# Optimization experiments

Hardware: AMD Instinct MI355X
Metric: run time of the kernel (lower is better)

Reference implementation:

```python
import jax, jax.numpy as jnp
import numpy as np

B, L, HID = 4, 1024, 1024
H, D = 16, 64  # num heads, head size


def setup_inputs() -> dict:
    key = jax.random.key(0)
    ks = jax.random.split(key, 12)
    s = 0.02
    return {
        "hidden_states": jax.random.normal(ks[0], (B, L, HID), jnp.float32),
        "attention_mask": jnp.zeros((B, 1, 1, L), jnp.float32),
        "structure_matrix": jax.random.normal(ks[1], (L, L, D), jnp.float32),
        # torch nn.Linear weights are [out, in]
        "Wq": jax.random.normal(ks[2], (H * D, HID), jnp.float32) * s,
        "bq": jnp.zeros((H * D,), jnp.float32),
        "Wk": jax.random.normal(ks[3], (H * D, HID), jnp.float32) * s,
        "bk": jnp.zeros((H * D,), jnp.float32),
        "Wv": jax.random.normal(ks[4], (H * D, HID), jnp.float32) * s,
        "bv": jnp.zeros((H * D,), jnp.float32),
        "Wsq": jax.random.normal(ks[5], (D, D), jnp.float32) * s,
        "bsq": jnp.zeros((D,), jnp.float32),
        "Wsk": jax.random.normal(ks[6], (D, D), jnp.float32) * s,
        "bsk": jnp.zeros((D,), jnp.float32),
    }


def _heads(x):
    # [B, L, H*D] -> [B, H, L, D]
    return x.reshape(B, L, H, D).transpose(0, 2, 1, 3)


def reference(hidden_states, attention_mask, structure_matrix,
              Wq, bq, Wk, bk, Wv, bv, Wsq, bsq, Wsk, bsk):
    q = _heads(hidden_states @ Wq.T + bq)  # [B,H,L,D]
    k = _heads(hidden_states @ Wk.T + bk)
    v = _heads(hidden_states @ Wv.T + bv)

    scores = jnp.einsum('bhld,bhrd->bhlr', q, k)

    sq = structure_matrix @ Wsq.T + bsq  # [L,L,D]
    sk = structure_matrix @ Wsk.T + bsk
    scores = scores + jnp.einsum('bhld,lrd->bhlr', q, sq) \
                    + jnp.einsum('bhrd,lrd->bhlr', k, sk)

    scores = scores / jnp.sqrt(jnp.float32(D)) + attention_mask
    probs = jax.nn.softmax(scores, axis=-1)
    ctx = jnp.einsum('bhlr,bhrd->bhld', probs, v)
    ctx = ctx.transpose(0, 2, 1, 3).reshape(B, L, H * D)
    return ctx, scores
```

## Files before the change

kernel.cpp:

```cpp
#include <hip/hip_runtime.h>

typedef __attribute__((ext_vector_type(8))) short short8v;
typedef __attribute__((ext_vector_type(4))) short short4v;
typedef __attribute__((ext_vector_type(4))) float float4v;
typedef __attribute__((ext_vector_type(2))) unsigned int uint2v;

#define MFMA16(a,b,c) __builtin_amdgcn_mfma_f32_16x16x32_bf16(a,b,c,0,0,0)

__device__ __forceinline__ unsigned short f2b(float f) {
    union { float f; unsigned u; } v; v.f = f;
    unsigned r = v.u + 0x7FFFu + ((v.u >> 16) & 1u);
    return (unsigned short)(r >> 16);
}
__device__ __forceinline__ float b2f(unsigned short s) {
    union { unsigned u; float f; } v; v.u = ((unsigned)s) << 16;
    return v.f;
}
__device__ __forceinline__ short8v pack8(float4v a, float4v b) {
    union { unsigned u[4]; short8v s; } o;
    asm("v_cvt_pk_bf16_f32 %0, %1, %2" : "=v"(o.u[0]) : "v"(a[0]), "v"(a[1]));
    asm("v_cvt_pk_bf16_f32 %0, %1, %2" : "=v"(o.u[1]) : "v"(a[2]), "v"(a[3]));
    asm("v_cvt_pk_bf16_f32 %0, %1, %2" : "=v"(o.u[2]) : "v"(b[0]), "v"(b[1]));
    asm("v_cvt_pk_bf16_f32 %0, %1, %2" : "=v"(o.u[3]) : "v"(b[2]), "v"(b[3]));
    return o.s;
}

__global__ __launch_bounds__(256) void pack_all(
    const float* __restrict__ hidden, const float* __restrict__ Wq,
    const float* __restrict__ Wk, const float* __restrict__ Wv,
    unsigned short* __restrict__ hb, unsigned short* __restrict__ Wqb,
    unsigned short* __restrict__ Wkb, unsigned short* __restrict__ Wvb) {
    const int bid = blockIdx.x;
    const float* in; unsigned short* out; int i;
    if (bid < 2048)      { in = hidden; out = hb;  i = bid * 256 + threadIdx.x; }
    else if (bid < 2560) { in = Wq; out = Wqb; i = (bid - 2048) * 256 + threadIdx.x; }
    else if (bid < 3072) { in = Wk; out = Wkb; i = (bid - 2560) * 256 + threadIdx.x; }
    else                 { in = Wv; out = Wvb; i = (bid - 3072) * 256 + threadIdx.x; }
    float4v a = *(const float4v*)&in[(size_t)i * 8];
    float4v b = *(const float4v*)&in[(size_t)i * 8 + 4];
    *(short8v*)&out[(size_t)i * 8] = pack8(a, b);
}

__global__ __launch_bounds__(256) void qkv_gemm(
    const unsigned short* __restrict__ A,
    const unsigned short* __restrict__ Wqb, const unsigned short* __restrict__ Wkb,
    const unsigned short* __restrict__ Wvb,
    const float* __restrict__ bq, const float* __restrict__ bk,
    const float* __restrict__ bv,
    unsigned short* __restrict__ outq) {
    const int n0g = blockIdx.x * 64;
    const int which = n0g >> 10;
    const int n0 = n0g & 1023;
    const unsigned short* W = (which == 0) ? Wqb : (which == 1) ? Wkb : Wvb;
    const float* bias = (which == 0) ? bq : (which == 1) ? bk : bv;
    unsigned short* out = outq + (size_t)which * 4194304;
    const int vmode = (which == 2);
    const int wave = threadIdx.x >> 6, lane = threadIdx.x & 63;
    const int m0 = blockIdx.y * 128 + wave * 32;
    const int lrow = lane & 15, g8 = (lane >> 4) << 3, row4 = (lane >> 4) << 2;
    float4v acc[2][4] = {};
    const unsigned short* Ap = A + (size_t)(m0 + lrow) * 1024 + g8;
    const unsigned short* Wp = W + (size_t)(n0 + lrow) * 1024 + g8;
#pragma unroll 2
    for (int k0 = 0; k0 < 1024; k0 += 32) {
        short8v a0 = *(const short8v*)(Ap + k0);
        short8v a1 = *(const short8v*)(Ap + 16 * 1024 + k0);
        short8v b0 = *(const short8v*)(Wp + k0);
        short8v b1 = *(const short8v*)(Wp + 16 * 1024 + k0);
        short8v b2 = *(const short8v*)(Wp + 32 * 1024 + k0);
        short8v b3 = *(const short8v*)(Wp + 48 * 1024 + k0);
        acc[0][0] = MFMA16(a0, b0, acc[0][0]); acc[0][1] = MFMA16(a0, b1, acc[0][1]);
        acc[0][2] = MFMA16(a0, b2, acc[0][2]); acc[0][3] = MFMA16(a0, b3, acc[0][3]);
        acc[1][0] = MFMA16(a1, b0, acc[1][0]); acc[1][1] = MFMA16(a1, b1, acc[1][1]);
        acc[1][2] = MFMA16(a1, b2, acc[1][2]); acc[1][3] = MFMA16(a1, b3, acc[1][3]);
    }
#pragma unroll
    for (int nt = 0; nt < 4; ++nt) {
        const int n = n0 + nt * 16 + lrow;
        const float bz = bias[n];
        const int h = n >> 6, d = n & 63;
#pragma unroll
        for (int mt = 0; mt < 2; ++mt) {
            const int mb = m0 + mt * 16 + row4;
            if (vmode == 0) {
#pragma unroll
                for (int j = 0; j < 4; ++j) {
                    const int m = mb + j;
                    const int b = m >> 10, l = m & 1023;
                    out[(((size_t)(b * 16 + h) << 10) + l) * 64 + d] = f2b(acc[mt][nt][j] + bz);
                }
            } else {
                const int b = mb >> 10, r = mb & 1023;
                short4v pk;
#pragma unroll
                for (int j = 0; j < 4; ++j) pk[j] = (short)f2b(acc[mt][nt][j] + bz);
                *(short4v*)&out[((((size_t)(b * 16 + h)) << 6) + d) * 1024 + r] = pk;
            }
        }
    }
}

__global__ __launch_bounds__(256) void headproj(
    const unsigned short* __restrict__ xh,
    const float* __restrict__ Wsx,
    const float* __restrict__ bsx,
    unsigned short* __restrict__ x2b,
    float* __restrict__ xbv) {
    __shared__ __align__(16) float Ws[64 * 64];
    __shared__ float bs[64];
    __shared__ __align__(16) unsigned short Xl[64 * 64];
    const int tid = threadIdx.x;
    const int l = blockIdx.x;
#pragma unroll
    for (int i = 0; i < 4; ++i)
        *(float4v*)&Ws[tid * 4 + i * 1024] = *(const float4v*)&Wsx[tid * 4 + i * 1024];
    if (tid < 64) bs[tid] = bsx[tid];
    {
        const int bhh = tid >> 2, dq = (tid & 3) * 16;
        const unsigned short* src = &xh[((size_t)bhh * 1024 + l) * 64 + dq];
        *(short8v*)&Xl[bhh * 64 + dq] = *(const short8v*)src;
        *(short8v*)&Xl[bhh * 64 + dq + 8] = *(const short8v*)(src + 8);
    }
    __syncthreads();
    const int bh = tid >> 2, e0 = (tid & 3) * 16;
    float acc[16] = {};
    float bacc = 0.f;
    for (int d = 0; d < 64; ++d) {
        const float xd = b2f(Xl[bh * 64 + d]);
        bacc += xd * bs[d];
        const float* wr = &Ws[d * 64 + e0];
#pragma unroll
        for (int e = 0; e < 16; e += 4) {
            float4v w = *(const float4v*)&wr[e];
            acc[e] += xd * w[0]; acc[e + 1] += xd * w[1];
            acc[e + 2] += xd * w[2]; acc[e + 3] += xd * w[3];
        }
    }
    short8v p0, p1;
#pragma unroll
    for (int e = 0; e < 8; ++e) { p0[e] = (short)f2b(acc[e]); p1[e] = (short)f2b(acc[e + 8]); }
    unsigned short* dst = &x2b[((size_t)l * 64 + bh) * 64 + e0];
    *(short8v*)dst = p0; *(short8v*)(dst + 8) = p1;
    if ((tid & 3) == 0) xbv[l * 64 + bh] = bacc;
}

__global__ __launch_bounds__(256, 4) void struct_fused(
    const float* __restrict__ S,
    const unsigned short* __restrict__ q2b,
    const unsigned short* __restrict__ k2b,
    const float* __restrict__ qbv,
    const float* __restrict__ kbv,
    unsigned short* __restrict__ sb) {
    __shared__ __align__(16) unsigned short Ssh[256 * 64];
    __shared__ __align__(16) unsigned short t3g[4][4][16][16];
    const int tid = threadIdx.x;
    const int w = tid >> 6, lane = tid & 63;
    const int lrow = lane & 15, g = lane >> 4;
    const int g8 = g << 3, row4 = g << 2;
    const int w16 = w << 4;
    const int r0 = blockIdx.x << 4, l0 = blockIdx.y << 4;

    {
        const int u = tid & 15, roff = tid >> 4;
        const float* gp = S + ((size_t)l0 * 1024 + r0 + roff) * 64 + u * 4;
        float4v f[16];
#pragma unroll
        for (int i = 0; i < 16; ++i)
            f[i] = *(const float4v*)(gp + (size_t)i * 65536);
#pragma unroll
        for (int i = 0; i < 16; ++i) {
            const int R = (i << 4) + roff;
            const int K3 = (roff ^ i) & 7;
            const int pu = u ^ (K3 << 1);
            union { unsigned uu[2]; uint2v v2; } o;
            asm("v_cvt_pk_bf16_f32 %0, %1, %2" : "=v"(o.uu[0]) : "v"(f[i][0]), "v"(f[i][1]));
            asm("v_cvt_pk_bf16_f32 %0, %1, %2" : "=v"(o.uu[1]) : "v"(f[i][2]), "v"(f[i][3]));
            *(uint2v*)&Ssh[(R << 6) + (pu << 2)] = o.v2;
        }
    }
    float kbreg[4];
#pragma unroll
    for (int j = 0; j < 4; ++j)
        kbreg[j] = kbv[(size_t)(r0 + row4 + j) * 64 + w16 + lrow];
    __syncthreads();

    float4v c3[16];
#pragma unroll
    for (int ri = 0; ri < 16; ++ri) {
        const int row = lrow * 16 + ri;
        const int key = (lrow ^ ri) & 7;
        short8v a0 = *(const short8v*)&Ssh[row * 64 + ((g ^ key) << 3)];
        short8v a1 = *(const short8v*)&Ssh[row * 64 + (((4 + g) ^ key) << 3)];
        const unsigned short* Bp = k2b + ((size_t)(r0 + ri) * 64 + w16 + lrow) * 64 + g8;
        short8v b0 = *(const short8v*)Bp;
        short8v b1 = *(const short8v*)(Bp + 32);
        float4v acc = {};
        acc = MFMA16(a0, b0, acc);
        acc = MFMA16(a1, b1, acc);
        c3[ri] = acc;
    }

#pragma unroll
    for (int G = 0; G < 4; ++G) {
        if (g == G) {
#pragma unroll
            for (int j = 0; j < 4; ++j) {
                float4v la{c3[0][j], c3[1][j], c3[2][j], c3[3][j]};
                float4v lb{c3[4][j], c3[5][j], c3[6][j], c3[7][j]};
                float4v ha{c3[8][j], c3[9][j], c3[10][j], c3[11][j]};
                float4v hb{c3[12][j], c3[13][j], c3[14][j], c3[15][j]};
                *(short8v*)&t3g[w][j][lrow][0] = pack8(la, lb);
                *(short8v*)&t3g[w][j][lrow][8] = pack8(ha, hb);
            }
        }
        asm volatile("s_waitcnt lgkmcnt(0)" ::: "memory");
#pragma unroll
        for (int lj = 0; lj < 4; ++lj) {
            const int li = (G << 2) + lj;
            const int row = li * 16 + lrow;
            const int key = (li ^ lrow) & 7;
            short8v a0 = *(const short8v*)&Ssh[row * 64 + ((g ^ key) << 3)];
            short8v a1 = *(const short8v*)&Ssh[row * 64 + (((4 + g) ^ key) << 3)];
            const unsigned short* Bp = q2b + ((size_t)(l0 + li) * 64 + w16 + lrow) * 64 + g8;
            short8v b0 = *(const short8v*)Bp;
            short8v b1 = *(const short8v*)(Bp + 32);
            float4v c2 = {};
            c2 = MFMA16(a0, b0, c2);
            c2 = MFMA16(a1, b1, c2);
            short4v t3v = *(const short4v*)&t3g[w][lj][lrow][row4];
            const float qb = qbv[(size_t)(l0 + li) * 64 + w16 + lrow];
            short4v outv;
#pragma unroll
            for (int j = 0; j < 4; ++j)
                outv[j] = (short)f2b(c2[j] + b2f((unsigned short)t3v[j]) + qb + kbreg[j]);
            *(short4v*)&sb[((size_t)(l0 + li) * 64 + w16 + lrow) * 1024 + r0 + row4] = outv;
        }
    }
}

__global__ __launch_bounds__(256) void flash_kernel(
    const unsigned short* __restrict__ qh,
    const unsigned short* __restrict__ kh,
    const unsigned short* __restrict__ vT,
    const unsigned short* __restrict__ sb,
    const float* __restrict__ mask,
    float* __restrict__ scores,
    float* __restrict__ ctx) {
    __shared__ __align__(16) unsigned short pL[2][4][2][16][64];
    const int bid = blockIdx.x;
    const int bh  = (bid & 7) * 8 + ((bid >> 3) & 7);
    const int seg = bid >> 6;
    const int tid = threadIdx.x, w = tid >> 6, lane = tid & 63;
    const int l0 = ((seg << 2) | w) << 5;
    const int b = bh >> 4, h = bh & 15;
    const int lam = lane & 15, g = lane >> 4, g8 = g << 3, g4 = g << 2;
    const int key = (lam & 7) << 1;

    short8v qf[2][2];
#pragma unroll
    for (int mt = 0; mt < 2; ++mt)
#pragma unroll
        for (int ks = 0; ks < 2; ++ks)
            qf[mt][ks] = *(const short8v*)&qh[((size_t)bh * 1024 + l0 + mt * 16 + lam) * 64 + ks * 32 + g8];
    const int myl[2] = { l0 + lam, l0 + 16 + lam };
    float mrun[2] = { -3e38f, -3e38f }, sden[2] = { 0.f, 0.f };
    float4v opv[2][4] = {};

    for (int rt = 0; rt < 16; ++rt) {
        const int r0 = rt << 6;
        const int pc = rt & 1;
        float4v sacc[2][4] = {};
#pragma unroll
        for (int rs = 0; rs < 4; ++rs)
#pragma unroll
            for (int ks = 0; ks < 2; ++ks) {
                short8v kf = *(const short8v*)&kh[((size_t)bh * 1024 + r0 + rs * 16 + lam) * 64 + ks * 32 + g8];
                sacc[0][rs] = MFMA16(kf, qf[0][ks], sacc[0][rs]);
                sacc[1][rs] = MFMA16(kf, qf[1][ks], sacc[1][rs]);
            }
        float s8[2][4][4];
        float mx[2] = { -3e38f, -3e38f };
#pragma unroll
        for (int rs = 0; rs < 4; ++rs) {
            float4v mk = *(const float4v*)&mask[(size_t)b * 1024 + r0 + rs * 16 + g4];
#pragma unroll
            for (int mt = 0; mt < 2; ++mt) {
                short4v sbv = *(const short4v*)&sb[((size_t)myl[mt] * 64 + bh) * 1024 + r0 + rs * 16 + g4];
                float4v o;
#pragma unroll
                for (int j = 0; j < 4; ++j) {
                    const float v = (sacc[mt][rs][j] + b2f((unsigned short)sbv[j])) * 0.125f + mk[j];
                    s8[mt][rs][j] = v; o[j] = v;
                    mx[mt] = fmaxf(mx[mt], v);
                }
                *(float4v*)&scores[((size_t)bh * 1024 + myl[mt]) * 1024 + r0 + rs * 16 + g4] = o;
            }
        }
#pragma unroll
        for (int mt = 0; mt < 2; ++mt) {
            float t = mx[mt];
            t = fmaxf(t, __shfl_xor(t, 16));
            t = fmaxf(t, __shfl_xor(t, 32));
            const float mn = fmaxf(mrun[mt], t);
            const float f = __expf(mrun[mt] - mn);
            mrun[mt] = mn;
            float ps = 0.f;
#pragma unroll
            for (int rs = 0; rs < 4; ++rs)
#pragma unroll
                for (int j = 0; j < 4; ++j) {
                    const float p = __expf(s8[mt][rs][j] - mn);
                    s8[mt][rs][j] = p; ps += p;
                }
            ps += __shfl_xor(ps, 16);
            ps += __shfl_xor(ps, 32);
            sden[mt] = sden[mt] * f + ps;
#pragma unroll
            for (int dt = 0; dt < 4; ++dt)
#pragma unroll
                for (int j = 0; j < 4; ++j) opv[mt][dt][j] *= f;
        }
#pragma unroll
        for (int mt = 0; mt < 2; ++mt)
#pragma unroll
            for (int rs = 0; rs < 4; ++rs) {
                union { unsigned uu[2]; uint2v v2; } o;
                asm("v_cvt_pk_bf16_f32 %0, %1, %2" : "=v"(o.uu[0]) : "v"(s8[mt][rs][0]), "v"(s8[mt][rs][1]));
                asm("v_cvt_pk_bf16_f32 %0, %1, %2" : "=v"(o.uu[1]) : "v"(s8[mt][rs][2]), "v"(s8[mt][rs][3]));
                const int unit = ((rs << 2) | g) ^ key;
                *(uint2v*)&pL[pc][w][mt][lam][unit << 2] = o.v2;
            }
#pragma unroll
        for (int ks = 0; ks < 2; ++ks) {
            const int u = (((ks << 3) | (g << 1)) ^ key) << 2;
            short8v pb0 = *(const short8v*)&pL[pc][w][0][lam][u];
            short8v pb1 = *(const short8v*)&pL[pc][w][1][lam][u];
#pragma unroll
            for (int dt = 0; dt < 4; ++dt) {
                short8v va = *(const short8v*)&vT[((size_t)bh * 64 + dt * 16 + lam) * 1024 + r0 + ks * 32 + g8];
                opv[0][dt] = MFMA16(va, pb0, opv[0][dt]);
                opv[1][dt] = MFMA16(va, pb1, opv[1][dt]);
            }
        }
    }
#pragma unroll
    for (int mt = 0; mt < 2; ++mt) {
        const float inv = 1.f / sden[mt];
#pragma unroll
        for (int dt = 0; dt < 4; ++dt) {
            float4v o;
#pragma unroll
            for (int j = 0; j < 4; ++j) o[j] = opv[mt][dt][j] * inv;
            *(float4v*)&ctx[((size_t)b * 1024 + myl[mt]) * 1024 + h * 64 + dt * 16 + g4] = o;
        }
    }
}

extern "C" void kernel_launch(void* const* d_in, const int* in_sizes, int n_in,
                              void* d_out, int out_size, void* d_ws, size_t ws_size,
                              hipStream_t stream) {
    (void)in_sizes; (void)n_in; (void)out_size; (void)ws_size;
    const float* hidden = (const float*)d_in[0];
    const float* mask   = (const float*)d_in[1];
    const float* S      = (const float*)d_in[2];
    const float* Wq  = (const float*)d_in[3];  const float* bq  = (const float*)d_in[4];
    const float* Wk  = (const float*)d_in[5];  const float* bk  = (const float*)d_in[6];
    const float* Wv  = (const float*)d_in[7];  const float* bv  = (const float*)d_in[8];
    const float* Wsq = (const float*)d_in[9];  const float* bsq = (const float*)d_in[10];
    const float* Wsk = (const float*)d_in[11]; const float* bsk = (const float*)d_in[12];

    float* ctx    = (float*)d_out;
    float* scores = ctx + (size_t)4 * 1024 * 1024;

    char* ws = (char*)d_ws;
    unsigned short* sbuf = (unsigned short*)ws;
    unsigned short* hb  = (unsigned short*)ws;
    unsigned short* Wqb = (unsigned short*)(ws + (8u << 20));
    unsigned short* Wkb = (unsigned short*)(ws + (10u << 20));
    unsigned short* Wvb = (unsigned short*)(ws + (12u << 20));
    unsigned short* qh  = (unsigned short*)(ws + (size_t)(128u) * 1024 * 1024);
    unsigned short* kh  = qh  + (size_t)4 * 1024 * 1024;
    unsigned short* vT  = kh  + (size_t)4 * 1024 * 1024;
    unsigned short* q2b = vT  + (size_t)4 * 1024 * 1024;
    unsigned short* k2b = q2b + (size_t)4 * 1024 * 1024;
    float* qbv = (float*)(k2b + (size_t)4 * 1024 * 1024);
    float* kbv = qbv + 65536;

    pack_all<<<3584, 256, 0, stream>>>(hidden, Wq, Wk, Wv, hb, Wqb, Wkb, Wvb);
    qkv_gemm<<<dim3(48, 32), 256, 0, stream>>>(hb, Wqb, Wkb, Wvb, bq, bk, bv, qh);
    headproj<<<1024, 256, 0, stream>>>(qh, Wsq, bsq, q2b, qbv);
    headproj<<<1024, 256, 0, stream>>>(kh, Wsk, bsk, k2b, kbv);
    struct_fused<<<dim3(64, 64), 256, 0, stream>>>(S, q2b, k2b, qbv, kbv, sbuf);
    flash_kernel<<<512, 256, 0, stream>>>(qh, kh, vT, sbuf, mask, scores, ctx);
}
```

Before: 539.1 us.

## Retile structure kernel to 32 l-rows per block and halve flash query tile

```diff
diff --git a/kernel.cpp b/kernel.cpp
--- a/kernel.cpp
+++ b/kernel.cpp
@@ -144,32 +144,33 @@
     if ((tid & 3) == 0) xbv[l * 64 + bh] = bacc;
 }
 
-__global__ __launch_bounds__(256, 4) void struct_fused(
+__global__ __launch_bounds__(256, 2) void struct_fused(
     const float* __restrict__ S,
     const unsigned short* __restrict__ q2b,
     const unsigned short* __restrict__ k2b,
     const float* __restrict__ qbv,
     const float* __restrict__ kbv,
     unsigned short* __restrict__ sb) {
-    __shared__ __align__(16) unsigned short Ssh[256 * 64];
+    __shared__ __align__(16) unsigned short Ssh[512 * 64];
     __shared__ __align__(16) unsigned short t3g[4][4][16][16];
     const int tid = threadIdx.x;
     const int w = tid >> 6, lane = tid & 63;
     const int lrow = lane & 15, g = lane >> 4;
     const int g8 = g << 3, row4 = g << 2;
-    const int w16 = w << 4;
-    const int r0 = blockIdx.x << 4, l0 = blockIdx.y << 4;
-
-    {
+    const int lh = w >> 1, bhh = w & 1;
+    const int r0 = blockIdx.x << 4, l0 = blockIdx.y << 5;
+
+#pragma unroll
+    for (int ph = 0; ph < 2; ++ph) {
         const int u = tid & 15, roff = tid >> 4;
-        const float* gp = S + ((size_t)l0 * 1024 + r0 + roff) * 64 + u * 4;
+        const float* gp = S + ((size_t)(l0 + ph * 16) * 1024 + r0 + roff) * 64 + u * 4;
         float4v f[16];
 #pragma unroll
         for (int i = 0; i < 16; ++i)
             f[i] = *(const float4v*)(gp + (size_t)i * 65536);
 #pragma unroll
         for (int i = 0; i < 16; ++i) {
-            const int R = (i << 4) + roff;
+            const int R = ph * 256 + (i << 4) + roff;
             const int K3 = (roff ^ i) & 7;
             const int pu = u ^ (K3 << 1);
             union { unsigned uu[2]; uint2v v2; } o;
@@ -178,67 +179,71 @@
             *(uint2v*)&Ssh[(R << 6) + (pu << 2)] = o.v2;
         }
     }
-    float kbreg[4];
-#pragma unroll
-    for (int j = 0; j < 4; ++j)
-        kbreg[j] = kbv[(size_t)(r0 + row4 + j) * 64 + w16 + lrow];
     __syncthreads();
 
-    float4v c3[16];
-#pragma unroll
-    for (int ri = 0; ri < 16; ++ri) {
-        const int row = lrow * 16 + ri;
-        const int key = (lrow ^ ri) & 7;
-        short8v a0 = *(const short8v*)&Ssh[row * 64 + ((g ^ key) << 3)];
-        short8v a1 = *(const short8v*)&Ssh[row * 64 + (((4 + g) ^ key) << 3)];
-        const unsigned short* Bp = k2b + ((size_t)(r0 + ri) * 64 + w16 + lrow) * 64 + g8;
-        short8v b0 = *(const short8v*)Bp;
-        short8v b1 = *(const short8v*)(Bp + 32);
-        float4v acc = {};
-        acc = MFMA16(a0, b0, acc);
-        acc = MFMA16(a1, b1, acc);
-        c3[ri] = acc;
-    }
-
-#pragma unroll
-    for (int G = 0; G < 4; ++G) {
-        if (g == G) {
-#pragma unroll
-            for (int j = 0; j < 4; ++j) {
-                float4v la{c3[0][j], c3[1][j], c3[2][j], c3[3][j]};
-                float4v lb{c3[4][j], c3[5][j], c3[6][j], c3[7][j]};
-                float4v ha{c3[8][j], c3[9][j], c3[10][j], c3[11][j]};
-                float4v hb{c3[12][j], c3[13][j], c3[14][j], c3[15][j]};
-                *(short8v*)&t3g[w][j][lrow][0] = pack8(la, lb);
-                *(short8v*)&t3g[w][j][lrow][8] = pack8(ha, hb);
-            }
-        }
-        asm volatile("s_waitcnt lgkmcnt(0)" ::: "memory");
-#pragma unroll
-        for (int lj = 0; lj < 4; ++lj) {
-            const int li = (G << 2) + lj;
-            const int row = li * 16 + lrow;
-            const int key = (li ^ lrow) & 7;
+#pragma unroll
+    for (int bhg = 0; bhg < 2; ++bhg) {
+        const int bhb = bhh * 32 + bhg * 16;
+        float kbreg[4];
+#pragma unroll
+        for (int j = 0; j < 4; ++j)
+            kbreg[j] = kbv[(size_t)(r0 + row4 + j) * 64 + bhb + lrow];
+        float4v c3[16];
+#pragma unroll
+        for (int ri = 0; ri < 16; ++ri) {
+            const int row = lh * 256 + lrow * 16 + ri;
+            const int key = (ri ^ lrow) & 7;
             short8v a0 = *(const short8v*)&Ssh[row * 64 + ((g ^ key) << 3)];
             short8v a1 = *(const short8v*)&Ssh[row * 64 + (((4 + g) ^ key) << 3)];
-            const unsigned short* Bp = q2b + ((size_t)(l0 + li) * 64 + w16 + lrow) * 64 + g8;
+            const unsigned short* Bp = k2b + ((size_t)(r0 + ri) * 64 + bhb + lrow) * 64 + g8;
             short8v b0 = *(const short8v*)Bp;
             short8v b1 = *(const short8v*)(Bp + 32);
-            float4v c2 = {};
-            c2 = MFMA16(a0, b0, c2);
-            c2 = MFMA16(a1, b1, c2);
-            short4v t3v = *(const short4v*)&t3g[w][lj][lrow][row4];
-            const float qb = qbv[(size_t)(l0 + li) * 64 + w16 + lrow];
-            short4v outv;
-#pragma unroll
-            for (int j = 0; j < 4; ++j)
-                outv[j] = (short)f2b(c2[j] + b2f((unsigned short)t3v[j]) + qb + kbreg[j]);
-            *(short4v*)&sb[((size_t)(l0 + li) * 64 + w16 + lrow) * 1024 + r0 + row4] = outv;
-        }
-    }
-}
-
-__global__ __launch_bounds__(256) void flash_kernel(
+            float4v acc = {};
+            acc = MFMA16(a0, b0, acc);
+            acc = MFMA16(a1, b1, acc);
+            c3[ri] = acc;
+        }
+#pragma unroll
+        for (int G = 0; G < 4; ++G) {
+            if (g == G) {
+#pragma unroll
+                for (int j = 0; j < 4; ++j) {
+                    float4v la{c3[0][j], c3[1][j], c3[2][j], c3[3][j]};
+                    float4v lb{c3[4][j], c3[5][j], c3[6][j], c3[7][j]};
+                    float4v ha{c3[8][j], c3[9][j], c3[10][j], c3[11][j]};
+                    float4v hb{c3[12][j], c3[13][j], c3[14][j], c3[15][j]};
+                    *(short8v*)&t3g[w][j][lrow][0] = pack8(la, lb);
+                    *(short8v*)&t3g[w][j][lrow][8] = pack8(ha, hb);
+                }
+            }
+            asm volatile("s_waitcnt lgkmcnt(0)" ::: "memory");
+#pragma unroll
+            for (int lj = 0; lj < 4; ++lj) {
+                const int li = (G << 2) + lj;
+                const int l = l0 + lh * 16 + li;
+                const int row = lh * 256 + li * 16 + lrow;
+                const int key = (li ^ lrow) & 7;
+                short8v a0 = *(const short8v*)&Ssh[row * 64 + ((g ^ key) << 3)];
+                short8v a1 = *(const short8v*)&Ssh[row * 64 + (((4 + g) ^ key) << 3)];
+                const unsigned short* Bp = q2b + ((size_t)l * 64 + bhb + lrow) * 64 + g8;
+                short8v b0 = *(const short8v*)Bp;
+                short8v b1 = *(const short8v*)(Bp + 32);
+                float4v c2 = {};
+                c2 = MFMA16(a0, b0, c2);
+                c2 = MFMA16(a1, b1, c2);
+                short4v t3v = *(const short4v*)&t3g[w][lj][lrow][row4];
+                const float qb = qbv[(size_t)l * 64 + bhb + lrow];
+                short4v outv;
+#pragma unroll
+                for (int j = 0; j < 4; ++j)
+                    outv[j] = (short)f2b(c2[j] + b2f((unsigned short)t3v[j]) + qb + kbreg[j]);
+                *(short4v*)&sb[((size_t)l * 64 + bhb + lrow) * 1024 + r0 + row4] = outv;
+            }
+        }
+    }
+}
+
+__global__ __launch_bounds__(256, 4) void flash_kernel(
     const unsigned short* __restrict__ qh,
     const unsigned short* __restrict__ kh,
     const unsigned short* __restrict__ vT,
@@ -246,112 +251,104 @@
     const float* __restrict__ mask,
     float* __restrict__ scores,
     float* __restrict__ ctx) {
-    __shared__ __align__(16) unsigned short pL[2][4][2][16][64];
+    __shared__ __align__(16) unsigned short pL[2][4][16][64];
     const int bid = blockIdx.x;
     const int bh  = (bid & 7) * 8 + ((bid >> 3) & 7);
     const int seg = bid >> 6;
     const int tid = threadIdx.x, w = tid >> 6, lane = tid & 63;
-    const int l0 = ((seg << 2) | w) << 5;
+    const int l0 = ((seg << 2) | w) << 4;
     const int b = bh >> 4, h = bh & 15;
     const int lam = lane & 15, g = lane >> 4, g8 = g << 3, g4 = g << 2;
     const int key = (lam & 7) << 1;
 
-    short8v qf[2][2];
-#pragma unroll
-    for (int mt = 0; mt < 2; ++mt)
-#pragma unroll
-        for (int ks = 0; ks < 2; ++ks)
-            qf[mt][ks] = *(const short8v*)&qh[((size_t)bh * 1024 + l0 + mt * 16 + lam) * 64 + ks * 32 + g8];
-    const int myl[2] = { l0 + lam, l0 + 16 + lam };
-    float mrun[2] = { -3e38f, -3e38f }, sden[2] = { 0.f, 0.f };
-    float4v opv[2][4] = {};
+    short8v qf[2];
+#pragma unroll
+    for (int ks = 0; ks < 2; ++ks)
+        qf[ks] = *(const short8v*)&qh[((size_t)bh * 1024 + l0 + lam) * 64 + ks * 32 + g8];
+    const int myl = l0 + lam;
+    float mrun = -3e38f, sden = 0.f;
+    float4v opv[4] = {};
 
     for (int rt = 0; rt < 16; ++rt) {
         const int r0 = rt << 6;
         const int pc = rt & 1;
-        float4v sacc[2][4] = {};
+        float4v sacc[4] = {};
+        __builtin_amdgcn_s_setprio(1);
 #pragma unroll
         for (int rs = 0; rs < 4; ++rs)
 #pragma unroll
             for (int ks = 0; ks < 2; ++ks) {
                 short8v kf = *(const short8v*)&kh[((size_t)bh * 1024 + r0 + rs * 16 + lam) * 64 + ks * 32 + g8];
-                sacc[0][rs] = MFMA16(kf, qf[0][ks], sacc[0][rs]);
-                sacc[1][rs] = MFMA16(kf, qf[1][ks], sacc[1][rs]);
-            }
-        float s8[2][4][4];
-        float mx[2] = { -3e38f, -3e38f };
+                sacc[rs] = MFMA16(kf, qf[ks], sacc[rs]);
+            }
+        __builtin_amdgcn_s_setprio(0);
+        float s8[4][4];
+        float mx = -3e38f;
 #pragma unroll
         for (int rs = 0; rs < 4; ++rs) {
             float4v mk = *(const float4v*)&mask[(size_t)b * 1024 + r0 + rs * 16 + g4];
-#pragma unroll
-            for (int mt = 0; mt < 2; ++mt) {
-                short4v sbv = *(const short4v*)&sb[((size_t)myl[mt] * 64 + bh) * 1024 + r0 + rs * 16 + g4];
-                float4v o;
-#pragma unroll
-                for (int j = 0; j < 4; ++j) {
-                    const float v = (sacc[mt][rs][j] + b2f((unsigned short)sbv[j])) * 0.125f + mk[j];
-                    s8[mt][rs][j] = v; o[j] = v;
-                    mx[mt] = fmaxf(mx[mt], v);
-                }
-                *(float4v*)&scores[((size_t)bh * 1024 + myl[mt]) * 1024 + r0 + rs * 16 + g4] = o;
-            }
-        }
-#pragma unroll
-        for (int mt = 0; mt < 2; ++mt) {
-            float t = mx[mt];
+            short4v sbv = *(const short4v*)&sb[((size_t)myl * 64 + bh) * 1024 + r0 + rs * 16 + g4];
+            float4v o;
+#pragma unroll
+            for (int j = 0; j < 4; ++j) {
+                const float v = (sacc[rs][j] + b2f((unsigned short)sbv[j])) * 0.125f + mk[j];
+                s8[rs][j] = v; o[j] = v;
+                mx = fmaxf(mx, v);
+            }
+            *(float4v*)&scores[((size_t)bh * 1024 + myl) * 1024 + r0 + rs * 16 + g4] = o;
+        }
+        {
+            float t = mx;
             t = fmaxf(t, __shfl_xor(t, 16));
             t = fmaxf(t, __shfl_xor(t, 32));
-            const float mn = fmaxf(mrun[mt], t);
-            const float f = __expf(mrun[mt] - mn);
-            mrun[mt] = mn;
+            const float mn = fmaxf(mrun, t);
+            const float f = __expf(mrun - mn);
+            mrun = mn;
             float ps = 0.f;
 #pragma unroll
             for (int rs = 0; rs < 4; ++rs)
 #pragma unroll
                 for (int j = 0; j < 4; ++j) {
-                    const float p = __expf(s8[mt][rs][j] - mn);
-                    s8[mt][rs][j] = p; ps += p;
+                    const float p = __expf(s8[rs][j] - mn);
+                    s8[rs][j] = p; ps += p;
                 }
             ps += __shfl_xor(ps, 16);
             ps += __shfl_xor(ps, 32);
-            sden[mt] = sden[mt] * f + ps;
+            sden = sden * f + ps;
 #pragma unroll
             for (int dt = 0; dt < 4; ++dt)
 #pragma unroll
-                for (int j = 0; j < 4; ++j) opv[mt][dt][j] *= f;
-        }
-#pragma unroll
-        for (int mt = 0; mt < 2; ++mt)
-#pragma unroll
-            for (int rs = 0; rs < 4; ++rs) {
-                union { unsigned uu[2]; uint2v v2; } o;
-                asm("v_cvt_pk_bf16_f32 %0, %1, %2" : "=v"(o.uu[0]) : "v"(s8[mt][rs][0]), "v"(s8[mt][rs][1]));
-                asm("v_cvt_pk_bf16_f32 %0, %1, %2" : "=v"(o.uu[1]) : "v"(s8[mt][rs][2]), "v"(s8[mt][rs][3]));
-                const int unit = ((rs << 2) | g) ^ key;
-                *(uint2v*)&pL[pc][w][mt][lam][unit << 2] = o.v2;
-            }
+                for (int j = 0; j < 4; ++j) opv[dt][j] *= f;
+        }
+#pragma unroll
+        for (int rs = 0; rs < 4; ++rs) {
+            union { unsigned uu[2]; uint2v v2; } o;
+            asm("v_cvt_pk_bf16_f32 %0, %1, %2" : "=v"(o.uu[0]) : "v"(s8[rs][0]), "v"(s8[rs][1]));
+            asm("v_cvt_pk_bf16_f32 %0, %1, %2" : "=v"(o.uu[1]) : "v"(s8[rs][2]), "v"(s8[rs][3]));
+            const int unit = ((rs << 2) | g) ^ key;
+            *(uint2v*)&pL[pc][w][lam][unit << 2] = o.v2;
+        }
 #pragma unroll
         for (int ks = 0; ks < 2; ++ks) {
             const int u = (((ks << 3) | (g << 1)) ^ key) << 2;
-            short8v pb0 = *(const short8v*)&pL[pc][w][0][lam][u];
-            short8v pb1 = *(const short8v*)&pL[pc][w][1][lam][u];
+            short8v pb = *(const short8v*)&pL[pc][w][lam][u];
+            __builtin_amdgcn_s_setprio(1);
 #pragma unroll
             for (int dt = 0; dt < 4; ++dt) {
                 short8v va = *(const short8v*)&vT[((size_t)bh * 64 + dt * 16 + lam) * 1024 + r0 + ks * 32 + g8];
-                opv[0][dt] = MFMA16(va, pb0, opv[0][dt]);
-                opv[1][dt] = MFMA16(va, pb1, opv[1][dt]);
-            }
-        }
-    }
-#pragma unroll
-    for (int mt = 0; mt < 2; ++mt) {
-        const float inv = 1.f / sden[mt];
+                opv[dt] = MFMA16(va, pb, opv[dt]);
+            }
+            __builtin_amdgcn_s_setprio(0);
+        }
+    }
+    {
+        const float inv = 1.f / sden;
 #pragma unroll
         for (int dt = 0; dt < 4; ++dt) {
             float4v o;
 #pragma unroll
-            for (int j = 0; j < 4; ++j) o[j] = opv[mt][dt][j] * inv;
-            *(float4v*)&ctx[((size_t)b * 1024 + myl[mt]) * 1024 + h * 64 + dt * 16 + g4] = o;
+            for (int j = 0; j < 4; ++j) o[j] = opv[dt][j] * inv;
+            *(float4v*)&ctx[((size_t)b * 1024 + myl) * 1024 + h * 64 + dt * 16 + g4] = o;
         }
     }
 }
@@ -390,6 +387,6 @@
     qkv_gemm<<<dim3(48, 32), 256, 0, stream>>>(hb, Wqb, Wkb, Wvb, bq, bk, bv, qh);
     headproj<<<1024, 256, 0, stream>>>(qh, Wsq, bsq, q2b, qbv);
     headproj<<<1024, 256, 0, stream>>>(kh, Wsk, bsk, k2b, kbv);
-    struct_fused<<<dim3(64, 64), 256, 0, stream>>>(S, q2b, k2b, qbv, kbv, sbuf);
-    flash_kernel<<<512, 256, 0, stream>>>(qh, kh, vT, sbuf, mask, scores, ctx);
-}
+    struct_fused<<<dim3(64, 32), 256, 0, stream>>>(S, q2b, k2b, qbv, kbv, sbuf);
+    flash_kernel<<<1024, 256, 0, stream>>>(qh, kh, vT, sbuf, mask, scores, ctx);
+}
```

Result: slower. 579.9 us (+7.6%).
